# Optimization experiments

Hardware: AMD Instinct MI355X
Metric: run time of the kernel (lower is better)

Reference implementation:

```python
import jax, jax.numpy as jnp
import numpy as np

LN_EPS = 1e-5
KERNEL_EPS = 1e-4


def layer_norm(x, gamma, beta):
    mu = jnp.mean(x, axis=-1, keepdims=True)
    var = jnp.mean((x - mu) ** 2, axis=-1, keepdims=True)
    return (x - mu) * jax.lax.rsqrt(var + LN_EPS) * gamma + beta


def softmax_kernel(data, proj, is_query):
    # Performer softmax random-feature map (performer-pytorch softmax_kernel)
    d = data.shape[-1]
    m = proj.shape[0]
    data_normalizer = d ** -0.25
    ratio = m ** -0.5
    # [B,H,S,D] x [M,D] -> [B,H,S,M]
    proj_data = jnp.einsum('bhnd,md->bhnm', data_normalizer * data, proj)
    diag = 0.5 * (data_normalizer ** 2) * jnp.sum(data * data, axis=-1, keepdims=True)
    if is_query:
        mx = jax.lax.stop_gradient(jnp.max(proj_data, axis=-1, keepdims=True))
    else:
        mx = jax.lax.stop_gradient(jnp.max(proj_data, axis=(-2, -1), keepdims=True))
    return ratio * (jnp.exp(proj_data - diag - mx) + KERNEL_EPS)


def setup_inputs() -> dict:
    key = jax.random.key(0)
    k1, k2 = jax.random.split(key)
    B, S, D, M, H = 4, 4096, 256, 256, 8
    x = jax.random.normal(k1, (B, S, D), dtype=jnp.float32)
    gamma = jnp.ones((D,), dtype=jnp.float32)
    beta = jnp.zeros((D,), dtype=jnp.float32)
    proj_matrix = jax.random.normal(k2, (M, D), dtype=jnp.float32)
    return {"x": x, "gamma": gamma, "beta": beta, "proj_matrix": proj_matrix, "num_heads": H}


def reference(x, gamma, beta, proj_matrix, num_heads):
    xn = layer_norm(x, gamma, beta)                       # [B,S,D]
    B, S, D = xn.shape
    h = jnp.broadcast_to(xn[:, None], (B, num_heads, S, D))  # stacked copies per head
    q = softmax_kernel(h, proj_matrix, True)              # [B,H,S,M]
    k = softmax_kernel(h, proj_matrix, False)             # [B,H,S,M]
    v = h                                                 # [B,H,S,D]
    # non-causal linear attention
    k_sum = jnp.sum(k, axis=-2)                           # [B,H,M]
    d_inv = 1.0 / jnp.einsum('bhnm,bhm->bhn', q, k_sum)   # [B,H,S]
    context = jnp.einsum('bhnm,bhnd->bhmd', k, v)         # [B,H,M,D]
    out = jnp.einsum('bhmd,bhnm,bhn->bhnd', context, q, d_inv)
    return out
```

## Files before the change

kernel.cpp:

```cpp
#include <hip/hip_runtime.h>
#include <math.h>

#define Bn 4
#define Hn 8
#define Sn 4096
#define Dn 256
#define Mn 256
#define BSn (Bn*Sn)
#define LN_EPS 1e-5f
#define KEPS 1e-4f
#define DATA_NORM 0.25f
#define RATIO 0.0625f

typedef short s8v __attribute__((ext_vector_type(8)));
typedef short s4v __attribute__((ext_vector_type(4)));
typedef float f4v __attribute__((ext_vector_type(4)));

#define BSTR 72

__device__ __forceinline__ unsigned short f2bf(float x) {
    unsigned u = __float_as_uint(x);
    u += 0x7FFFu + ((u >> 16) & 1u);
    return (unsigned short)(u >> 16);
}
__device__ __forceinline__ float bf2f(unsigned short h) {
    return __uint_as_float(((unsigned)h) << 16);
}
__device__ __forceinline__ unsigned enc_f(float f) {
    unsigned u = __float_as_uint(f);
    return (u & 0x80000000u) ? ~u : (u | 0x80000000u);
}
__device__ __forceinline__ float dec_f(unsigned u) {
    unsigned b = (u & 0x80000000u) ? (u ^ 0x80000000u) : ~u;
    return __uint_as_float(b);
}

__device__ __forceinline__ float blockReduceMax(float v) {
    __shared__ float buf[4];
    #pragma unroll
    for (int o = 32; o > 0; o >>= 1) v = fmaxf(v, __shfl_down(v, o));
    __syncthreads();
    if ((threadIdx.x & 63) == 0) buf[threadIdx.x >> 6] = v;
    __syncthreads();
    return fmaxf(fmaxf(buf[0], buf[1]), fmaxf(buf[2], buf[3]));
}

__device__ __forceinline__ void stage_bf16(const unsigned short* base, int ld,
                                           unsigned short* L, int t) {
    const int row = t >> 1, c0 = (t & 1) * 32;
    const unsigned short* p = base + (size_t)row * ld + c0;
    #pragma unroll
    for (int q = 0; q < 4; q++)
        *(s8v*)&L[row * BSTR + c0 + q * 8] = *(const s8v*)&p[q * 8];
}

__device__ __forceinline__ void mfma_step64(const unsigned short* A, const unsigned short* B,
                                            int wr, int wc, int lane, f4v acc[4][4]) {
    const int quad = lane >> 4, r = lane & 15;
    #pragma unroll
    for (int ks = 0; ks < 2; ks++) {
        s8v a[4], b[4];
        #pragma unroll
        for (int i = 0; i < 4; i++) {
            a[i] = *(const s8v*)&A[(wr * 64 + i * 16 + r) * BSTR + ks * 32 + quad * 8];
            b[i] = *(const s8v*)&B[(wc * 64 + i * 16 + r) * BSTR + ks * 32 + quad * 8];
        }
        #pragma unroll
        for (int i = 0; i < 4; i++)
            #pragma unroll
            for (int j = 0; j < 4; j++)
                acc[i][j] = __builtin_amdgcn_mfma_f32_16x16x32_bf16(a[i], b[j], acc[i][j], 0, 0, 0);
    }
}

__global__ __launch_bounds__(256) void k_splitp(const float* __restrict__ P,
                                                unsigned short* __restrict__ Ph,
                                                unsigned short* __restrict__ Pl) {
    const int i = (blockIdx.x * 256 + threadIdx.x) * 8;
    float v[8];
    *(float4*)&v[0] = *(const float4*)&P[i];
    *(float4*)&v[4] = *(const float4*)&P[i + 4];
    s8v hh, ll;
    #pragma unroll
    for (int e = 0; e < 8; e++) {
        unsigned short h = f2bf(v[e]);
        hh[e] = (short)h;
        ll[e] = (short)f2bf(v[e] - bf2f(h));
    }
    *(s8v*)&Ph[i] = hh;
    *(s8v*)&Pl[i] = ll;
}

__global__ __launch_bounds__(256) void k_ln(const float* __restrict__ X,
                                            const float* __restrict__ gamma,
                                            const float* __restrict__ beta,
                                            unsigned short* __restrict__ XNh,
                                            unsigned short* __restrict__ XNl,
                                            float* __restrict__ diag,
                                            unsigned* __restrict__ mxqI) {
    const int w = threadIdx.x >> 6, l = threadIdx.x & 63;
    const int row = blockIdx.x * 4 + w;
    float4 x = *(const float4*)&X[(size_t)row * Dn + l * 4];
    float s = x.x + x.y + x.z + x.w;
    #pragma unroll
    for (int o = 32; o > 0; o >>= 1) s += __shfl_xor(s, o);
    const float mean = s * (1.0f / Dn);
    float xn[4] = {x.x - mean, x.y - mean, x.z - mean, x.w - mean};
    float vs = xn[0] * xn[0] + xn[1] * xn[1] + xn[2] * xn[2] + xn[3] * xn[3];
    #pragma unroll
    for (int o = 32; o > 0; o >>= 1) vs += __shfl_xor(vs, o);
    const float rs = rsqrtf(vs * (1.0f / Dn) + LN_EPS);
    float4 g = *(const float4*)&gamma[l * 4];
    float4 bt = *(const float4*)&beta[l * 4];
    xn[0] = xn[0] * rs * g.x + bt.x;
    xn[1] = xn[1] * rs * g.y + bt.y;
    xn[2] = xn[2] * rs * g.z + bt.z;
    xn[3] = xn[3] * rs * g.w + bt.w;
    s4v hv, lv;
    float d2 = 0.0f;
    #pragma unroll
    for (int c = 0; c < 4; c++) {
        d2 += xn[c] * xn[c];
        unsigned short h = f2bf(xn[c]);
        hv[c] = (short)h;
        lv[c] = (short)f2bf(xn[c] - bf2f(h));
    }
    *(s4v*)&XNh[(size_t)row * Dn + l * 4] = hv;
    *(s4v*)&XNl[(size_t)row * Dn + l * 4] = lv;
    #pragma unroll
    for (int o = 32; o > 0; o >>= 1) d2 += __shfl_xor(d2, o);
    if (l == 0) { diag[row] = 0.03125f * d2; mxqI[row] = 0u; }
}

__global__ __launch_bounds__(256, 2) void k_gemm1(const unsigned short* __restrict__ XNh,
                                                  const unsigned short* __restrict__ XNl,
                                                  const unsigned short* __restrict__ Ph,
                                                  const unsigned short* __restrict__ Pl,
                                                  float* __restrict__ PD,
                                                  unsigned* __restrict__ mxqI) {
    __shared__ unsigned short Ah[64 * BSTR], Al[64 * BSTR];
    __shared__ unsigned short Bh[128 * BSTR], Bl[128 * BSTR];
    const int t = threadIdx.x, lane = t & 63, w = t >> 6;
    const int wr = w >> 1, wc = w & 1, quad = lane >> 4, cc = lane & 15;
    const int r0 = blockIdx.x * 64, m0 = blockIdx.y * 128;
    const int ar0 = t >> 3, ac8 = (t & 7) * 8;
    f4v acc[2][4];
    #pragma unroll
    for (int i = 0; i < 2; i++)
        #pragma unroll
        for (int j = 0; j < 4; j++)
            #pragma unroll
            for (int r = 0; r < 4; r++) acc[i][j][r] = 0.0f;

    for (int kt = 0; kt < Dn; kt += 64) {
        __syncthreads();
        *(s8v*)&Ah[ar0 * BSTR + ac8]        = *(const s8v*)&XNh[(size_t)(r0 + ar0) * Dn + kt + ac8];
        *(s8v*)&Al[ar0 * BSTR + ac8]        = *(const s8v*)&XNl[(size_t)(r0 + ar0) * Dn + kt + ac8];
        *(s8v*)&Ah[(ar0 + 32) * BSTR + ac8] = *(const s8v*)&XNh[(size_t)(r0 + ar0 + 32) * Dn + kt + ac8];
        *(s8v*)&Al[(ar0 + 32) * BSTR + ac8] = *(const s8v*)&XNl[(size_t)(r0 + ar0 + 32) * Dn + kt + ac8];
        #pragma unroll
        for (int ss = 0; ss < 4; ss++) {
            const int row = ar0 + ss * 32;
            *(s8v*)&Bh[row * BSTR + ac8] = *(const s8v*)&Ph[(size_t)(m0 + row) * Dn + kt + ac8];
            *(s8v*)&Bl[row * BSTR + ac8] = *(const s8v*)&Pl[(size_t)(m0 + row) * Dn + kt + ac8];
        }
        __syncthreads();
        #pragma unroll
        for (int ks = 0; ks < 2; ks++) {
            s8v ah[2], al[2], bh[4], bl[4];
            #pragma unroll
            for (int i = 0; i < 2; i++) {
                const int m = wr * 32 + i * 16 + cc;
                ah[i] = *(const s8v*)&Ah[m * BSTR + ks * 32 + quad * 8];
                al[i] = *(const s8v*)&Al[m * BSTR + ks * 32 + quad * 8];
            }
            #pragma unroll
            for (int j = 0; j < 4; j++) {
                const int n = wc * 64 + j * 16 + cc;
                bh[j] = *(const s8v*)&Bh[n * BSTR + ks * 32 + quad * 8];
                bl[j] = *(const s8v*)&Bl[n * BSTR + ks * 32 + quad * 8];
            }
            #pragma unroll
            for (int i = 0; i < 2; i++)
                #pragma unroll
                for (int j = 0; j < 4; j++) {
                    acc[i][j] = __builtin_amdgcn_mfma_f32_16x16x32_bf16(ah[i], bh[j], acc[i][j], 0, 0, 0);
                    acc[i][j] = __builtin_amdgcn_mfma_f32_16x16x32_bf16(ah[i], bl[j], acc[i][j], 0, 0, 0);
                    acc[i][j] = __builtin_amdgcn_mfma_f32_16x16x32_bf16(al[i], bh[j], acc[i][j], 0, 0, 0);
                }
        }
    }
    float rmax[2][4];
    #pragma unroll
    for (int i = 0; i < 2; i++)
        #pragma unroll
        for (int r = 0; r < 4; r++) rmax[i][r] = -INFINITY;
    #pragma unroll
    for (int i = 0; i < 2; i++) {
        const int row = r0 + wr * 32 + i * 16 + quad * 4;
        #pragma unroll
        for (int j = 0; j < 4; j++) {
            const int col = m0 + wc * 64 + j * 16 + cc;
            #pragma unroll
            for (int r = 0; r < 4; r++) {
                float v = DATA_NORM * acc[i][j][r];
                PD[(size_t)(row + r) * Mn + col] = v;
                rmax[i][r] = fmaxf(rmax[i][r], v);
            }
        }
    }
    #pragma unroll
    for (int i = 0; i < 2; i++)
        #pragma unroll
        for (int r = 0; r < 4; r++) {
            float v = rmax[i][r];
            v = fmaxf(v, __shfl_xor(v, 1));
            v = fmaxf(v, __shfl_xor(v, 2));
            v = fmaxf(v, __shfl_xor(v, 4));
            v = fmaxf(v, __shfl_xor(v, 8));
            if (cc == 0)
                atomicMax(&mxqI[r0 + wr * 32 + i * 16 + quad * 4 + r], enc_f(v));
        }
}

__global__ __launch_bounds__(256) void k_batchmax(const unsigned* __restrict__ mxqI,
                                                  float* __restrict__ mxqF,
                                                  float* __restrict__ mxk,
                                                  float* __restrict__ KSUM) {
    const int b = blockIdx.x;
    KSUM[b * Mn + threadIdx.x] = 0.0f;
    float m = -INFINITY;
    for (int i = threadIdx.x; i < Sn; i += 256) {
        float f = dec_f(mxqI[b * Sn + i]);
        mxqF[b * Sn + i] = f;
        m = fmaxf(m, f);
    }
    m = blockReduceMax(m);
    if (threadIdx.x == 0) mxk[b] = m;
}

__global__ __launch_bounds__(256) void k_featvt(const float* __restrict__ PD,
                                                const unsigned short* __restrict__ XNh,
                                                const float* __restrict__ diag,
                                                const float* __restrict__ mxk,
                                                const float* __restrict__ mxqF,
                                                unsigned short* __restrict__ KT,
                                                unsigned short* __restrict__ QR,
                                                unsigned short* __restrict__ VT,
                                                float* __restrict__ KSUM) {
    const int s0 = blockIdx.x * 64, c0 = blockIdx.y * 64, z = blockIdx.z;
    const int t = threadIdx.x;
    const int sr = t >> 2, cc16 = (t & 3) * 16;
    if (z < 4) {
        __shared__ float T[64][65];
        const int b = z;
        const int gr = b * Sn + s0 + sr;
        const float dmv = diag[gr] + mxk[b];
        const float srow = __expf(mxk[b] - mxqF[gr]);
        const float* p = PD + (size_t)gr * Mn + c0 + cc16;
        float v[16];
        *(float4*)&v[0]  = *(const float4*)&p[0];
        *(float4*)&v[4]  = *(const float4*)&p[4];
        *(float4*)&v[8]  = *(const float4*)&p[8];
        *(float4*)&v[12] = *(const float4*)&p[12];
        s8v q0, q1;
        #pragma unroll
        for (int e = 0; e < 16; e++) {
            float ev = __expf(v[e] - dmv);
            T[cc16 + e][sr] = RATIO * (ev + KEPS);
            unsigned short qb = f2bf(RATIO * (ev * srow + KEPS));
            if (e < 8) q0[e] = (short)qb; else q1[e - 8] = (short)qb;
        }
        *(s8v*)&QR[(size_t)gr * Mn + c0 + cc16]     = q0;
        *(s8v*)&QR[(size_t)gr * Mn + c0 + cc16 + 8] = q1;
        __syncthreads();
        const int ml = t >> 2, sc = (t & 3) * 16;
        float ks = 0.0f;
        s8v o0, o1;
        #pragma unroll
        for (int i = 0; i < 8; i++) {
            float f0 = T[ml][sc + i], f1 = T[ml][sc + 8 + i];
            ks += f0 + f1;
            o0[i] = (short)f2bf(f0);
            o1[i] = (short)f2bf(f1);
        }
        unsigned short* q = KT + ((size_t)b * Mn + c0 + ml) * Sn + s0 + sc;
        *(s8v*)&q[0] = o0;
        *(s8v*)&q[8] = o1;
        ks += __shfl_xor(ks, 1);
        ks += __shfl_xor(ks, 2);
        if ((t & 3) == 0) atomicAdd(&KSUM[b * Mn + c0 + ml], ks);
    } else {
        __shared__ unsigned short Tu[64][72];
        const int b = z - 4;
        const int gr = b * Sn + s0 + sr;
        const unsigned short* p = XNh + (size_t)gr * Dn + c0 + cc16;
        s8v x0 = *(const s8v*)&p[0], x1 = *(const s8v*)&p[8];
        #pragma unroll
        for (int e = 0; e < 8; e++) {
            Tu[cc16 + e][sr]     = (unsigned short)x0[e];
            Tu[cc16 + 8 + e][sr] = (unsigned short)x1[e];
        }
        __syncthreads();
        const int dl = t >> 2, sc = (t & 3) * 16;
        s8v o0, o1;
        #pragma unroll
        for (int i = 0; i < 8; i++) {
            o0[i] = (short)Tu[dl][sc + i];
            o1[i] = (short)Tu[dl][sc + 8 + i];
        }
        unsigned short* q = VT + ((size_t)b * Dn + c0 + dl) * Sn + s0 + sc;
        *(s8v*)&q[0] = o0;
        *(s8v*)&q[8] = o1;
    }
}

__global__ __launch_bounds__(256, 2) void k_gemm2(const unsigned short* __restrict__ VT,
                                                  const unsigned short* __restrict__ KT,
                                                  float* __restrict__ PART) {
    __shared__ unsigned short Abuf[128 * BSTR], Bbuf[128 * BSTR];
    const int t = threadIdx.x, lane = t & 63, w = t >> 6;
    const int wr = w >> 1, wc = w & 1, quad = lane >> 4, cc = lane & 15;
    const int chunk = blockIdx.x, til = blockIdx.y, b = blockIdx.z;
    const int d0 = (til >> 1) * 128, m0 = (til & 1) * 128;
    const unsigned short* Ab = VT + ((size_t)b * Dn + d0) * Sn + chunk * 256;
    const unsigned short* Bb = KT + ((size_t)b * Mn + m0) * Sn + chunk * 256;
    f4v acc[4][4];
    #pragma unroll
    for (int i = 0; i < 4; i++)
        #pragma unroll
        for (int j = 0; j < 4; j++)
            #pragma unroll
            for (int r = 0; r < 4; r++) acc[i][j][r] = 0.0f;

    for (int kt = 0; kt < 256; kt += 64) {
        __syncthreads();
        stage_bf16(Ab + kt, Sn, Abuf, t);
        stage_bf16(Bb + kt, Sn, Bbuf, t);
        __syncthreads();
        mfma_step64(Abuf, Bbuf, wr, wc, lane, acc);
    }
    float* dst = PART + (size_t)(chunk * Bn + b) * (Dn * Mn);
    #pragma unroll
    for (int i = 0; i < 4; i++) {
        const int drow = d0 + wr * 64 + i * 16 + quad * 4;
        #pragma unroll
        for (int j = 0; j < 4; j++) {
            const int col = m0 + wc * 64 + j * 16 + cc;
            #pragma unroll
            for (int r = 0; r < 4; r++)
                dst[(size_t)(drow + r) * Mn + col] = acc[i][j][r];
        }
    }
}

__global__ __launch_bounds__(256) void k_ctxred(const float* __restrict__ PART,
                                                unsigned short* __restrict__ CT) {
    const int g = blockIdx.x * 256 + threadIdx.x;
    float4 s = make_float4(0.f, 0.f, 0.f, 0.f);
    #pragma unroll
    for (int c = 0; c < 16; c++) {
        float4 p = *(const float4*)&PART[(size_t)c * 262144 + (size_t)g * 4];
        s.x += p.x; s.y += p.y; s.z += p.z; s.w += p.w;
    }
    s4v o;
    o[0] = (short)f2bf(s.x); o[1] = (short)f2bf(s.y);
    o[2] = (short)f2bf(s.z); o[3] = (short)f2bf(s.w);
    *(s4v*)&CT[(size_t)g * 4] = o;
}

__global__ __launch_bounds__(256, 2) void k_gemm3(const unsigned short* __restrict__ QR,
                                                  const unsigned short* __restrict__ CT,
                                                  const float* __restrict__ KSUM,
                                                  float* __restrict__ OUT) {
    __shared__ unsigned short Abuf[64 * BSTR], Bbuf[128 * BSTR];
    __shared__ float kslds[Mn];
    __shared__ float dinvS[64];
    const int t = threadIdx.x, lane = t & 63, w = t >> 6;
    const int wr = w >> 1, wc = w & 1, quad = lane >> 4, cc = lane & 15;
    const int r0 = blockIdx.x * 64, d0 = blockIdx.y * 128;
    const int b = r0 >> 12;
    kslds[t] = KSUM[b * Mn + t];
    const int ar0 = t >> 3, ac8 = (t & 7) * 8;
    float qks0 = 0.0f, qks1 = 0.0f;
    f4v acc[2][4];
    #pragma unroll
    for (int i = 0; i < 2; i++)
        #pragma unroll
        for (int j = 0; j < 4; j++)
            #pragma unroll
            for (int r = 0; r < 4; r++) acc[i][j][r] = 0.0f;

    for (int kt = 0; kt < Mn; kt += 64) {
        __syncthreads();
        s8v a0 = *(const s8v*)&QR[(size_t)(r0 + ar0) * Mn + kt + ac8];
        s8v a1 = *(const s8v*)&QR[(size_t)(r0 + ar0 + 32) * Mn + kt + ac8];
        *(s8v*)&Abuf[ar0 * BSTR + ac8]        = a0;
        *(s8v*)&Abuf[(ar0 + 32) * BSTR + ac8] = a1;
        #pragma unroll
        for (int e = 0; e < 8; e++) {
            const float ks = kslds[kt + ac8 + e];
            qks0 += bf2f((unsigned short)a0[e]) * ks;
            qks1 += bf2f((unsigned short)a1[e]) * ks;
        }
        #pragma unroll
        for (int ss = 0; ss < 4; ss++) {
            const int row = ar0 + ss * 32;
            *(s8v*)&Bbuf[row * BSTR + ac8] =
                *(const s8v*)&CT[((size_t)b * Dn + d0 + row) * Mn + kt + ac8];
        }
        __syncthreads();
        #pragma unroll
        for (int ks = 0; ks < 2; ks++) {
            s8v a[2], bb[4];
            #pragma unroll
            for (int i = 0; i < 2; i++)
                a[i] = *(const s8v*)&Abuf[(wr * 32 + i * 16 + cc) * BSTR + ks * 32 + quad * 8];
            #pragma unroll
            for (int j = 0; j < 4; j++)
                bb[j] = *(const s8v*)&Bbuf[(wc * 64 + j * 16 + cc) * BSTR + ks * 32 + quad * 8];
            #pragma unroll
            for (int i = 0; i < 2; i++)
                #pragma unroll
                for (int j = 0; j < 4; j++)
                    acc[i][j] = __builtin_amdgcn_mfma_f32_16x16x32_bf16(a[i], bb[j], acc[i][j], 0, 0, 0);
        }
    }
    qks0 += __shfl_xor(qks0, 1); qks0 += __shfl_xor(qks0, 2); qks0 += __shfl_xor(qks0, 4);
    qks1 += __shfl_xor(qks1, 1); qks1 += __shfl_xor(qks1, 2); qks1 += __shfl_xor(qks1, 4);
    if ((t & 7) == 0) {
        dinvS[ar0]      = 1.0f / qks0;
        dinvS[ar0 + 32] = 1.0f / qks1;
    }
    __syncthreads();
    #pragma unroll
    for (int i = 0; i < 2; i++) {
        const int rl0 = wr * 32 + i * 16 + quad * 4;
        #pragma unroll
        for (int r = 0; r < 4; r++) {
            const int rl = rl0 + r;
            const int gr = r0 + rl;
            const float dv = dinvS[rl];
            const int ss = gr & (Sn - 1);
            const size_t base = ((size_t)(b * Hn) * Sn + ss) * Dn;
            #pragma unroll
            for (int j = 0; j < 4; j++) {
                const int col = d0 + wc * 64 + j * 16 + cc;
                const float val = acc[i][j][r] * dv;
                #pragma unroll
                for (int h = 0; h < Hn; h++)
                    OUT[base + (size_t)h * Sn * Dn + col] = val;
            }
        }
    }
}

extern "C" void kernel_launch(void* const* d_in, const int* in_sizes, int n_in,
                              void* d_out, int out_size, void* d_ws, size_t ws_size,
                              hipStream_t stream) {
    const float* X     = (const float*)d_in[0];
    const float* gamma = (const float*)d_in[1];
    const float* beta  = (const float*)d_in[2];
    const float* P     = (const float*)d_in[3];
    float* OUT = (float*)d_out;

    char* base = (char*)d_ws;
    unsigned short* XNh = (unsigned short*)(base);
    unsigned short* XNl = (unsigned short*)(base + 8388608);
    float*          PD  = (float*)(base + 16777216);
    unsigned short* QR  = (unsigned short*)(base + 33554432);
    unsigned short* VT  = (unsigned short*)(base + 41943040);
    unsigned short* CT  = (unsigned short*)(base + 50331648);
    unsigned short* Ph  = (unsigned short*)(base + 50855936);
    unsigned short* Pl  = (unsigned short*)(base + 50987008);
    float*          diag = (float*)(base + 51118080);
    unsigned*       mxqI = (unsigned*)(base + 51183616);
    float*          mxqF = (float*)(base + 51249152);
    float*          mxk  = (float*)(base + 51314688);
    float*          KSUM = (float*)(base + 51314944);
    unsigned short* KT   = XNl;
    float*          PART = PD;

    k_splitp<<<32, 256, 0, stream>>>(P, Ph, Pl);
    k_ln<<<BSn / 4, 256, 0, stream>>>(X, gamma, beta, XNh, XNl, diag, mxqI);
    k_gemm1<<<dim3(BSn / 64, Mn / 128), 256, 0, stream>>>(XNh, XNl, Ph, Pl, PD, mxqI);
    k_batchmax<<<Bn, 256, 0, stream>>>(mxqI, mxqF, mxk, KSUM);
    k_featvt<<<dim3(Sn / 64, 4, 8), 256, 0, stream>>>(PD, XNh, diag, mxk, mxqF, KT, QR, VT, KSUM);
    k_gemm2<<<dim3(16, 4, Bn), 256, 0, stream>>>(VT, KT, PART);
    k_ctxred<<<256, 256, 0, stream>>>(PART, CT);
    k_gemm3<<<dim3(BSn / 64, Dn / 128), 256, 0, stream>>>(QR, CT, KSUM, OUT);
}
```

Before: 208.7 us.

## Fuse split/batchmax kernels, retile context GEMM, and coalesce output stores

```diff
diff --git a/kernel.cpp b/kernel.cpp
--- a/kernel.cpp
+++ b/kernel.cpp
@@ -35,69 +35,43 @@
     return __uint_as_float(b);
 }
 
-__device__ __forceinline__ float blockReduceMax(float v) {
-    __shared__ float buf[4];
-    #pragma unroll
-    for (int o = 32; o > 0; o >>= 1) v = fmaxf(v, __shfl_down(v, o));
-    __syncthreads();
-    if ((threadIdx.x & 63) == 0) buf[threadIdx.x >> 6] = v;
-    __syncthreads();
-    return fmaxf(fmaxf(buf[0], buf[1]), fmaxf(buf[2], buf[3]));
-}
-
-__device__ __forceinline__ void stage_bf16(const unsigned short* base, int ld,
-                                           unsigned short* L, int t) {
-    const int row = t >> 1, c0 = (t & 1) * 32;
-    const unsigned short* p = base + (size_t)row * ld + c0;
-    #pragma unroll
-    for (int q = 0; q < 4; q++)
-        *(s8v*)&L[row * BSTR + c0 + q * 8] = *(const s8v*)&p[q * 8];
-}
-
-__device__ __forceinline__ void mfma_step64(const unsigned short* A, const unsigned short* B,
-                                            int wr, int wc, int lane, f4v acc[4][4]) {
-    const int quad = lane >> 4, r = lane & 15;
-    #pragma unroll
-    for (int ks = 0; ks < 2; ks++) {
-        s8v a[4], b[4];
-        #pragma unroll
-        for (int i = 0; i < 4; i++) {
-            a[i] = *(const s8v*)&A[(wr * 64 + i * 16 + r) * BSTR + ks * 32 + quad * 8];
-            b[i] = *(const s8v*)&B[(wc * 64 + i * 16 + r) * BSTR + ks * 32 + quad * 8];
-        }
-        #pragma unroll
-        for (int i = 0; i < 4; i++)
-            #pragma unroll
-            for (int j = 0; j < 4; j++)
-                acc[i][j] = __builtin_amdgcn_mfma_f32_16x16x32_bf16(a[i], b[j], acc[i][j], 0, 0, 0);
-    }
-}
-
-__global__ __launch_bounds__(256) void k_splitp(const float* __restrict__ P,
-                                                unsigned short* __restrict__ Ph,
-                                                unsigned short* __restrict__ Pl) {
-    const int i = (blockIdx.x * 256 + threadIdx.x) * 8;
-    float v[8];
-    *(float4*)&v[0] = *(const float4*)&P[i];
-    *(float4*)&v[4] = *(const float4*)&P[i + 4];
-    s8v hh, ll;
-    #pragma unroll
-    for (int e = 0; e < 8; e++) {
-        unsigned short h = f2bf(v[e]);
-        hh[e] = (short)h;
-        ll[e] = (short)f2bf(v[e] - bf2f(h));
-    }
-    *(s8v*)&Ph[i] = hh;
-    *(s8v*)&Pl[i] = ll;
-}
-
 __global__ __launch_bounds__(256) void k_ln(const float* __restrict__ X,
                                             const float* __restrict__ gamma,
                                             const float* __restrict__ beta,
+                                            const float* __restrict__ P,
                                             unsigned short* __restrict__ XNh,
                                             unsigned short* __restrict__ XNl,
+                                            unsigned short* __restrict__ Ph,
+                                            unsigned short* __restrict__ Pl,
                                             float* __restrict__ diag,
-                                            unsigned* __restrict__ mxqI) {
+                                            unsigned* __restrict__ mxqI,
+                                            float* __restrict__ KSUM,
+                                            unsigned* __restrict__ mxkI) {
+    if (blockIdx.x >= BSn / 4) {
+        const int e = blockIdx.x - BSn / 4;
+        if (e < 32) {
+            const int i = (e * 256 + threadIdx.x) * 8;
+            float v[8];
+            *(float4*)&v[0] = *(const float4*)&P[i];
+            *(float4*)&v[4] = *(const float4*)&P[i + 4];
+            s8v hh, ll;
+            #pragma unroll
+            for (int q = 0; q < 8; q++) {
+                unsigned short h = f2bf(v[q]);
+                hh[q] = (short)h;
+                ll[q] = (short)f2bf(v[q] - bf2f(h));
+            }
+            *(s8v*)&Ph[i] = hh;
+            *(s8v*)&Pl[i] = ll;
+        } else {
+            KSUM[threadIdx.x]       = 0.0f;
+            KSUM[threadIdx.x + 256] = 0.0f;
+            KSUM[threadIdx.x + 512] = 0.0f;
+            KSUM[threadIdx.x + 768] = 0.0f;
+            if (threadIdx.x < 4) mxkI[threadIdx.x] = 0u;
+        }
+        return;
+    }
     const int w = threadIdx.x >> 6, l = threadIdx.x & 63;
     const int row = blockIdx.x * 4 + w;
     float4 x = *(const float4*)&X[(size_t)row * Dn + l * 4];
@@ -137,9 +111,11 @@
                                                   const unsigned short* __restrict__ Ph,
                                                   const unsigned short* __restrict__ Pl,
                                                   float* __restrict__ PD,
-                                                  unsigned* __restrict__ mxqI) {
+                                                  unsigned* __restrict__ mxqI,
+                                                  unsigned* __restrict__ mxkI) {
     __shared__ unsigned short Ah[64 * BSTR], Al[64 * BSTR];
     __shared__ unsigned short Bh[128 * BSTR], Bl[128 * BSTR];
+    __shared__ float bmS[4];
     const int t = threadIdx.x, lane = t & 63, w = t >> 6;
     const int wr = w >> 1, wc = w & 1, quad = lane >> 4, cc = lane & 15;
     const int r0 = blockIdx.x * 64, m0 = blockIdx.y * 128;
@@ -221,29 +197,21 @@
             if (cc == 0)
                 atomicMax(&mxqI[r0 + wr * 32 + i * 16 + quad * 4 + r], enc_f(v));
         }
-}
-
-__global__ __launch_bounds__(256) void k_batchmax(const unsigned* __restrict__ mxqI,
-                                                  float* __restrict__ mxqF,
-                                                  float* __restrict__ mxk,
-                                                  float* __restrict__ KSUM) {
-    const int b = blockIdx.x;
-    KSUM[b * Mn + threadIdx.x] = 0.0f;
-    float m = -INFINITY;
-    for (int i = threadIdx.x; i < Sn; i += 256) {
-        float f = dec_f(mxqI[b * Sn + i]);
-        mxqF[b * Sn + i] = f;
-        m = fmaxf(m, f);
-    }
-    m = blockReduceMax(m);
-    if (threadIdx.x == 0) mxk[b] = m;
+    float bm = fmaxf(fmaxf(rmax[0][0], rmax[0][1]), fmaxf(rmax[0][2], rmax[0][3]));
+    bm = fmaxf(bm, fmaxf(fmaxf(rmax[1][0], rmax[1][1]), fmaxf(rmax[1][2], rmax[1][3])));
+    #pragma unroll
+    for (int o = 32; o > 0; o >>= 1) bm = fmaxf(bm, __shfl_xor(bm, o));
+    if (lane == 0) bmS[w] = bm;
+    __syncthreads();
+    if (t == 0)
+        atomicMax(&mxkI[r0 >> 12], enc_f(fmaxf(fmaxf(bmS[0], bmS[1]), fmaxf(bmS[2], bmS[3]))));
 }
 
 __global__ __launch_bounds__(256) void k_featvt(const float* __restrict__ PD,
                                                 const unsigned short* __restrict__ XNh,
                                                 const float* __restrict__ diag,
-                                                const float* __restrict__ mxk,
-                                                const float* __restrict__ mxqF,
+                                                const unsigned* __restrict__ mxkI,
+                                                const unsigned* __restrict__ mxqI,
                                                 unsigned short* __restrict__ KT,
                                                 unsigned short* __restrict__ QR,
                                                 unsigned short* __restrict__ VT,
@@ -255,8 +223,9 @@
         __shared__ float T[64][65];
         const int b = z;
         const int gr = b * Sn + s0 + sr;
-        const float dmv = diag[gr] + mxk[b];
-        const float srow = __expf(mxk[b] - mxqF[gr]);
+        const float mk = dec_f(mxkI[b]);
+        const float dmv = diag[gr] + mk;
+        const float srow = __expf(mk - dec_f(mxqI[gr]));
         const float* p = PD + (size_t)gr * Mn + c0 + cc16;
         float v[16];
         *(float4*)&v[0]  = *(const float4*)&p[0];
@@ -318,35 +287,52 @@
 __global__ __launch_bounds__(256, 2) void k_gemm2(const unsigned short* __restrict__ VT,
                                                   const unsigned short* __restrict__ KT,
                                                   float* __restrict__ PART) {
-    __shared__ unsigned short Abuf[128 * BSTR], Bbuf[128 * BSTR];
+    __shared__ unsigned short Abuf[64 * BSTR], Bbuf[64 * BSTR];
     const int t = threadIdx.x, lane = t & 63, w = t >> 6;
     const int wr = w >> 1, wc = w & 1, quad = lane >> 4, cc = lane & 15;
     const int chunk = blockIdx.x, til = blockIdx.y, b = blockIdx.z;
-    const int d0 = (til >> 1) * 128, m0 = (til & 1) * 128;
-    const unsigned short* Ab = VT + ((size_t)b * Dn + d0) * Sn + chunk * 256;
-    const unsigned short* Bb = KT + ((size_t)b * Mn + m0) * Sn + chunk * 256;
-    f4v acc[4][4];
-    #pragma unroll
-    for (int i = 0; i < 4; i++)
-        #pragma unroll
-        for (int j = 0; j < 4; j++)
+    const int d0 = (til >> 2) * 64, m0 = (til & 3) * 64;
+    const unsigned short* Ab = VT + ((size_t)b * Dn + d0) * Sn + chunk * 1024;
+    const unsigned short* Bb = KT + ((size_t)b * Mn + m0) * Sn + chunk * 1024;
+    const int sr = t >> 2, sc = (t & 3) * 16;
+    f4v acc[2][2];
+    #pragma unroll
+    for (int i = 0; i < 2; i++)
+        #pragma unroll
+        for (int j = 0; j < 2; j++)
             #pragma unroll
             for (int r = 0; r < 4; r++) acc[i][j][r] = 0.0f;
 
-    for (int kt = 0; kt < 256; kt += 64) {
-        __syncthreads();
-        stage_bf16(Ab + kt, Sn, Abuf, t);
-        stage_bf16(Bb + kt, Sn, Bbuf, t);
-        __syncthreads();
-        mfma_step64(Abuf, Bbuf, wr, wc, lane, acc);
+    for (int kt = 0; kt < 1024; kt += 64) {
+        __syncthreads();
+        *(s8v*)&Abuf[sr * BSTR + sc]     = *(const s8v*)&Ab[(size_t)sr * Sn + kt + sc];
+        *(s8v*)&Abuf[sr * BSTR + sc + 8] = *(const s8v*)&Ab[(size_t)sr * Sn + kt + sc + 8];
+        *(s8v*)&Bbuf[sr * BSTR + sc]     = *(const s8v*)&Bb[(size_t)sr * Sn + kt + sc];
+        *(s8v*)&Bbuf[sr * BSTR + sc + 8] = *(const s8v*)&Bb[(size_t)sr * Sn + kt + sc + 8];
+        __syncthreads();
+        #pragma unroll
+        for (int ks = 0; ks < 2; ks++) {
+            s8v a[2], bb[2];
+            #pragma unroll
+            for (int i = 0; i < 2; i++)
+                a[i] = *(const s8v*)&Abuf[(wr * 32 + i * 16 + cc) * BSTR + ks * 32 + quad * 8];
+            #pragma unroll
+            for (int j = 0; j < 2; j++)
+                bb[j] = *(const s8v*)&Bbuf[(wc * 32 + j * 16 + cc) * BSTR + ks * 32 + quad * 8];
+            #pragma unroll
+            for (int i = 0; i < 2; i++)
+                #pragma unroll
+                for (int j = 0; j < 2; j++)
+                    acc[i][j] = __builtin_amdgcn_mfma_f32_16x16x32_bf16(a[i], bb[j], acc[i][j], 0, 0, 0);
+        }
     }
     float* dst = PART + (size_t)(chunk * Bn + b) * (Dn * Mn);
     #pragma unroll
-    for (int i = 0; i < 4; i++) {
-        const int drow = d0 + wr * 64 + i * 16 + quad * 4;
-        #pragma unroll
-        for (int j = 0; j < 4; j++) {
-            const int col = m0 + wc * 64 + j * 16 + cc;
+    for (int i = 0; i < 2; i++) {
+        const int drow = d0 + wr * 32 + i * 16 + quad * 4;
+        #pragma unroll
+        for (int j = 0; j < 2; j++) {
+            const int col = m0 + wc * 32 + j * 16 + cc;
             #pragma unroll
             for (int r = 0; r < 4; r++)
                 dst[(size_t)(drow + r) * Mn + col] = acc[i][j][r];
@@ -359,7 +345,7 @@
     const int g = blockIdx.x * 256 + threadIdx.x;
     float4 s = make_float4(0.f, 0.f, 0.f, 0.f);
     #pragma unroll
-    for (int c = 0; c < 16; c++) {
+    for (int c = 0; c < 4; c++) {
         float4 p = *(const float4*)&PART[(size_t)c * 262144 + (size_t)g * 4];
         s.x += p.x; s.y += p.y; s.z += p.z; s.w += p.w;
     }
@@ -376,6 +362,7 @@
     __shared__ unsigned short Abuf[64 * BSTR], Bbuf[128 * BSTR];
     __shared__ float kslds[Mn];
     __shared__ float dinvS[64];
+    __shared__ float OutS[64][136];
     const int t = threadIdx.x, lane = t & 63, w = t >> 6;
     const int wr = w >> 1, wc = w & 1, quad = lane >> 4, cc = lane & 15;
     const int r0 = blockIdx.x * 64, d0 = blockIdx.y * 128;
@@ -438,20 +425,25 @@
         const int rl0 = wr * 32 + i * 16 + quad * 4;
         #pragma unroll
         for (int r = 0; r < 4; r++) {
-            const int rl = rl0 + r;
-            const int gr = r0 + rl;
-            const float dv = dinvS[rl];
-            const int ss = gr & (Sn - 1);
-            const size_t base = ((size_t)(b * Hn) * Sn + ss) * Dn;
-            #pragma unroll
-            for (int j = 0; j < 4; j++) {
-                const int col = d0 + wc * 64 + j * 16 + cc;
-                const float val = acc[i][j][r] * dv;
-                #pragma unroll
-                for (int h = 0; h < Hn; h++)
-                    OUT[base + (size_t)h * Sn * Dn + col] = val;
-            }
-        }
+            const float dv = dinvS[rl0 + r];
+            #pragma unroll
+            for (int j = 0; j < 4; j++)
+                OutS[rl0 + r][wc * 64 + j * 16 + cc] = acc[i][j][r] * dv;
+        }
+    }
+    __syncthreads();
+    const int rb = t >> 5;
+    const int c4 = (t & 31) * 4;
+    #pragma unroll
+    for (int it = 0; it < 8; it++) {
+        const int row = it * 8 + rb;
+        float4 v = *(const float4*)&OutS[row][c4];
+        const int gr = r0 + row;
+        const int ss = gr & (Sn - 1);
+        const size_t basep = ((size_t)(b * Hn) * Sn + ss) * Dn + d0 + c4;
+        #pragma unroll
+        for (int h = 0; h < Hn; h++)
+            *(float4*)&OUT[basep + (size_t)h * Sn * Dn] = v;
     }
 }
 
@@ -475,18 +467,15 @@
     unsigned short* Pl  = (unsigned short*)(base + 50987008);
     float*          diag = (float*)(base + 51118080);
     unsigned*       mxqI = (unsigned*)(base + 51183616);
-    float*          mxqF = (float*)(base + 51249152);
-    float*          mxk  = (float*)(base + 51314688);
+    unsigned*       mxkI = (unsigned*)(base + 51314688);
     float*          KSUM = (float*)(base + 51314944);
     unsigned short* KT   = XNl;
     float*          PART = PD;
 
-    k_splitp<<<32, 256, 0, stream>>>(P, Ph, Pl);
-    k_ln<<<BSn / 4, 256, 0, stream>>>(X, gamma, beta, XNh, XNl, diag, mxqI);
-    k_gemm1<<<dim3(BSn / 64, Mn / 128), 256, 0, stream>>>(XNh, XNl, Ph, Pl, PD, mxqI);
-    k_batchmax<<<Bn, 256, 0, stream>>>(mxqI, mxqF, mxk, KSUM);
-    k_featvt<<<dim3(Sn / 64, 4, 8), 256, 0, stream>>>(PD, XNh, diag, mxk, mxqF, KT, QR, VT, KSUM);
-    k_gemm2<<<dim3(16, 4, Bn), 256, 0, stream>>>(VT, KT, PART);
+    k_ln<<<BSn / 4 + 33, 256, 0, stream>>>(X, gamma, beta, P, XNh, XNl, Ph, Pl, diag, mxqI, KSUM, mxkI);
+    k_gemm1<<<dim3(BSn / 64, Mn / 128), 256, 0, stream>>>(XNh, XNl, Ph, Pl, PD, mxqI, mxkI);
+    k_featvt<<<dim3(Sn / 64, 4, 8), 256, 0, stream>>>(PD, XNh, diag, mxkI, mxqI, KT, QR, VT, KSUM);
+    k_gemm2<<<dim3(4, 16, Bn), 256, 0, stream>>>(VT, KT, PART);
     k_ctxred<<<256, 256, 0, stream>>>(PART, CT);
     k_gemm3<<<dim3(BSn / 64, Dn / 128), 256, 0, stream>>>(QR, CT, KSUM, OUT);
 }
```

Result: no change. 205.0 us (-1.8%).
